# Optimization experiments

Measured on AMD Instinct MI355X. Metric: run time of the kernel, lower is better.

Reference implementation:

```python
import math
import jax, jax.numpy as jnp
import numpy as np

N = 100000
E = 3200000
NFEAT = 128
NHID = 128
NCLASS = 40
NLAYERS = 8
LAMDA = 0.5
ALPHA = 0.1


def setup_inputs() -> dict:
    key = jax.random.key(0)
    ks = jax.random.split(key, 8)
    x = jax.random.normal(ks[0], (N, NFEAT), dtype=jnp.float32)
    edge_src = jax.random.randint(ks[1], (E,), 0, N, dtype=jnp.int32)
    edge_dst = jax.random.randint(ks[2], (E,), 0, N, dtype=jnp.int32)
    # positive normalized-adjacency-like values
    edge_val = jax.random.uniform(ks[3], (E,), dtype=jnp.float32) * 0.05
    W_in = jax.random.normal(ks[4], (NFEAT, NHID), dtype=jnp.float32) * (1.0 / math.sqrt(NFEAT))
    b_in = jnp.zeros((NHID,), dtype=jnp.float32)
    conv_w = jax.random.normal(ks[5], (NLAYERS, NHID, NHID), dtype=jnp.float32) * (1.0 / math.sqrt(NHID))
    W_out = jax.random.normal(ks[6], (NHID, NCLASS), dtype=jnp.float32) * (1.0 / math.sqrt(NHID))
    b_out = jnp.zeros((NCLASS,), dtype=jnp.float32)
    return {"x": x, "edge_src": edge_src, "edge_dst": edge_dst, "edge_val": edge_val,
            "W_in": W_in, "b_in": b_in, "conv_w": conv_w, "W_out": W_out, "b_out": b_out}


def _spmm(edge_src, edge_dst, edge_val, h):
    # sparse adj @ h : gather source rows, scale by edge weight, scatter-add to dst
    msgs = edge_val[:, None] * h[edge_src]          # [E, NHID]
    return jax.ops.segment_sum(msgs, edge_dst, num_segments=N)


def reference(x, edge_src, edge_dst, edge_val, W_in, b_in, conv_w, W_out, b_out):
    h0 = x @ W_in + b_in                            # fc_in (dropout = identity in eval)
    h = h0
    for i in range(NLAYERS):
        layer_idx = i + 1
        theta = math.log(LAMDA / layer_idx + 1.0)
        hi = _spmm(edge_src, edge_dst, edge_val, h)  # [N, NHID]
        support = (1.0 - ALPHA) * hi + ALPHA * h0    # convex combine with initial residual
        out = theta * (support @ conv_w[i]) + (1.0 - theta) * support  # identity mapping mix
        h = jax.nn.relu(out)
    return h @ W_out + b_out                         # fc_out
```

## Files before the change

### kernel.cpp

```cpp
#include <hip/hip_runtime.h>
#include <hip/hip_fp16.h>


constexpr int NN = 100000;
constexpr int EE = 3200000;
constexpr int NB = 256;
constexpr int NBUCK = (NN + 511) / 512;

struct alignas(8) Half4 { __half2 lo, hi; };

__global__ __launch_bounds__(256) void bhist_kernel(const int* __restrict__ dst,
                                                    int* __restrict__ bhist, int e) {
    __shared__ int lh[NB];
    lh[threadIdx.x] = 0;
    __syncthreads();
    for (int i = blockIdx.x * 256 + threadIdx.x; i < e; i += gridDim.x * 256)
        atomicAdd(&lh[dst[i] >> 9], 1);
    __syncthreads();
    if (lh[threadIdx.x]) atomicAdd(&bhist[threadIdx.x], lh[threadIdx.x]);
}

__global__ void bscan_kernel(const int* __restrict__ bhist, int* __restrict__ bbase,
                             int* __restrict__ bcur, int* __restrict__ row_ptr) {
    if (threadIdx.x == 0) {
        int s = 0;
        for (int b = 0; b < NB; ++b) { bbase[b] = s; bcur[b] = s; s += bhist[b]; }
        bbase[NB] = s;
        row_ptr[NN] = s;
    }
}

__global__ __launch_bounds__(256, 3) void bucket_kernel(const int* __restrict__ src,
                                                        const int* __restrict__ dst,
                                                        const float* __restrict__ val,
                                                        int* __restrict__ bcur,
                                                        int2* __restrict__ bsorted,
                                                        int* __restrict__ bdst, int e_total) {
    __shared__ int bin_cnt[NB], bin_excl[NB], bin_gbase[NB], bin_cur[NB];
    __shared__ int2 s_ed[4096];
    __shared__ int  s_dp[4096];
    const int tid = threadIdx.x;
    const int e_base = blockIdx.x * 4096;
    const int count = min(4096, e_total - e_base);
    bin_cnt[tid] = 0;
    __syncthreads();
    #pragma unroll
    for (int i = 0; i < 16; ++i) {
        int idx = e_base + i * 256 + tid;
        if (idx < e_total) atomicAdd(&bin_cnt[dst[idx] >> 9], 1);
    }
    __syncthreads();
    if (tid == 0) {
        int s = 0;
        for (int b = 0; b < NB; ++b) { bin_excl[b] = s; s += bin_cnt[b]; }
    }
    __syncthreads();
    bin_gbase[tid] = atomicAdd(&bcur[tid], bin_cnt[tid]);
    bin_cur[tid] = bin_excl[tid];
    __syncthreads();
    #pragma unroll
    for (int i = 0; i < 16; ++i) {
        int idx = e_base + i * 256 + tid;
        if (idx < e_total) {
            int d = dst[idx];
            int pos = atomicAdd(&bin_cur[d >> 9], 1);
            s_ed[pos] = make_int2(src[idx], __float_as_int(val[idx]));
            s_dp[pos] = d;
        }
    }
    __syncthreads();
    for (int pos = tid; pos < count; pos += 256) {
        int d = s_dp[pos], b = d >> 9;
        int g = bin_gbase[b] + (pos - bin_excl[b]);
        bsorted[g] = s_ed[pos];
        bdst[g] = d;
    }
}

__global__ __launch_bounds__(512) void finalize_kernel(const int2* __restrict__ bsorted,
                                                       const int* __restrict__ bdst,
                                                       const int* __restrict__ bbase,
                                                       int* __restrict__ row_ptr,
                                                       int2* __restrict__ csr) {
    __shared__ int hist[512], cur[512], wsum[8];
    const int tid = threadIdx.x, lane = tid & 63, wid = tid >> 6;
    const int b = blockIdx.x;
    const int n0 = b << 9;
    const int nodes = min(512, NN - n0);
    const int es = bbase[b], ee = bbase[b + 1], cnt = ee - es;
    hist[tid] = 0;
    __syncthreads();
    for (int i = tid; i < cnt; i += 512) atomicAdd(&hist[bdst[es + i] - n0], 1);
    __syncthreads();
    int v = hist[tid];
    int x = v;
    #pragma unroll
    for (int d = 1; d < 64; d <<= 1) {
        int y = __shfl_up(x, (unsigned)d);
        if (lane >= d) x += y;
    }
    if (lane == 63) wsum[wid] = x;
    __syncthreads();
    if (tid == 0) {
        int s = 0;
        for (int w = 0; w < 8; ++w) { int t2 = wsum[w]; wsum[w] = s; s += t2; }
    }
    __syncthreads();
    int excl = x - v + wsum[wid];
    cur[tid] = excl;
    if (tid < nodes) row_ptr[n0 + tid] = es + excl;
    __syncthreads();
    for (int i = tid; i < cnt; i += 512) {
        int d = bdst[es + i];
        int p = atomicAdd(&cur[d - n0], 1);
        csr[es + p] = bsorted[es + i];
    }
}

__global__ void prep_wc_kernel(const float* __restrict__ conv_w, float* __restrict__ Wc) {
    int layer = blockIdx.y;
    int idx = blockIdx.x * 256 + threadIdx.x;
    float theta = logf(0.5f / (float)(layer + 1) + 1.0f);
    int k = idx >> 7, j = idx & 127;
    float w = conv_w[layer * 16384 + idx];
    Wc[layer * 16384 + idx] = theta * w + ((k == j) ? (1.0f - theta) : 0.0f);
}

__global__ __launch_bounds__(256, 2) void fc_in_kernel(const float* __restrict__ x,
                                                       const float* __restrict__ W,
                                                       const float* __restrict__ b,
                                                       __half* __restrict__ h0) {
    __shared__ float sW[128 * 128];
    __shared__ float sA[32 * 128];
    const int tid = threadIdx.x;
    #pragma unroll
    for (int t = 0; t < 16; ++t)
        ((float4*)sW)[t * 256 + tid] = ((const float4*)W)[t * 256 + tid];
    const float4* xs = (const float4*)(x + (size_t)blockIdx.x * 32 * 128);
    #pragma unroll
    for (int t = 0; t < 4; ++t)
        ((float4*)sA)[t * 256 + tid] = xs[t * 256 + tid];
    __syncthreads();

    const int rowg = tid >> 5, colg = tid & 31;
    float4 bias = ((const float4*)b)[colg];
    float acc[4][4];
    #pragma unroll
    for (int r = 0; r < 4; ++r) { acc[r][0] = bias.x; acc[r][1] = bias.y; acc[r][2] = bias.z; acc[r][3] = bias.w; }

    for (int k = 0; k < 128; ++k) {
        float4 w = *(const float4*)&sW[k * 128 + (colg << 2)];
        float s[4];
        #pragma unroll
        for (int r = 0; r < 4; ++r) s[r] = sA[((rowg << 2) + r) * 128 + k];
        #pragma unroll
        for (int r = 0; r < 4; ++r) {
            acc[r][0] = fmaf(s[r], w.x, acc[r][0]);
            acc[r][1] = fmaf(s[r], w.y, acc[r][1]);
            acc[r][2] = fmaf(s[r], w.z, acc[r][2]);
            acc[r][3] = fmaf(s[r], w.w, acc[r][3]);
        }
    }
    const int row0 = blockIdx.x * 32;
    #pragma unroll
    for (int r = 0; r < 4; ++r) {
        Half4 o;
        o.lo = __floats2half2_rn(acc[r][0], acc[r][1]);
        o.hi = __floats2half2_rn(acc[r][2], acc[r][3]);
        *(Half4*)(h0 + ((size_t)(row0 + (rowg << 2) + r) << 7) + (colg << 2)) = o;
    }
}

#define FMA4(ACC, PV, G) { \
    float vv_ = __int_as_float((PV).y); \
    float2 lo_ = __half22float2((G).lo), hi_ = __half22float2((G).hi); \
    (ACC).x = fmaf(vv_, lo_.x, (ACC).x); (ACC).y = fmaf(vv_, lo_.y, (ACC).y); \
    (ACC).z = fmaf(vv_, hi_.x, (ACC).z); (ACC).w = fmaf(vv_, hi_.y, (ACC).w); }

__global__ __launch_bounds__(256, 8) void layer_kernel(const __half* __restrict__ h,
                                                       const __half* __restrict__ h0,
                                                       const int2* __restrict__ csr,
                                                       const int* __restrict__ row_ptr,
                                                       const float* __restrict__ Wc,
                                                       __half* __restrict__ hn) {
    __shared__ float sS[32 * 128];
    const int tid = threadIdx.x;
    const int wid = tid >> 6, lane = tid & 63;
    const int sub = lane >> 5;
    const int q4 = (lane & 31) << 2;
    const int row0 = blockIdx.x * 32;
    const int rb = __builtin_amdgcn_readfirstlane(row0 + wid * 8);

    for (int rr = 0; rr < 8; ++rr) {
        const int r = rb + rr;
        const int e0 = row_ptr[r], e1 = row_ptr[r + 1];
        float4 accA = make_float4(0.f, 0.f, 0.f, 0.f);
        float4 accB = make_float4(0.f, 0.f, 0.f, 0.f);
        int e = e0;
        for (; e + 16 <= e1; e += 16) {
            int2 c0 = csr[e + 0],  c1 = csr[e + 1],  c2 = csr[e + 2],  c3 = csr[e + 3];
            int2 c4 = csr[e + 4],  c5 = csr[e + 5],  c6 = csr[e + 6],  c7 = csr[e + 7];
            int2 c8 = csr[e + 8],  c9 = csr[e + 9],  c10 = csr[e + 10], c11 = csr[e + 11];
            int2 c12 = csr[e + 12], c13 = csr[e + 13], c14 = csr[e + 14], c15 = csr[e + 15];
            int2 p0 = sub ? c1 : c0;
            int2 p1 = sub ? c3 : c2;
            int2 p2 = sub ? c5 : c4;
            int2 p3 = sub ? c7 : c6;
            int2 p4 = sub ? c9 : c8;
            int2 p5 = sub ? c11 : c10;
            int2 p6 = sub ? c13 : c12;
            int2 p7 = sub ? c15 : c14;
            Half4 g0 = *(const Half4*)(h + ((size_t)p0.x << 7) + q4);
            Half4 g1 = *(const Half4*)(h + ((size_t)p1.x << 7) + q4);
            Half4 g2 = *(const Half4*)(h + ((size_t)p2.x << 7) + q4);
            Half4 g3 = *(const Half4*)(h + ((size_t)p3.x << 7) + q4);
            Half4 g4 = *(const Half4*)(h + ((size_t)p4.x << 7) + q4);
            Half4 g5 = *(const Half4*)(h + ((size_t)p5.x << 7) + q4);
            Half4 g6 = *(const Half4*)(h + ((size_t)p6.x << 7) + q4);
            Half4 g7 = *(const Half4*)(h + ((size_t)p7.x << 7) + q4);
            FMA4(accA, p0, g0); FMA4(accB, p1, g1);
            FMA4(accA, p2, g2); FMA4(accB, p3, g3);
            FMA4(accA, p4, g4); FMA4(accB, p5, g5);
            FMA4(accA, p6, g6); FMA4(accB, p7, g7);
        }
        if (e < e1) {
            #pragma unroll
            for (int k = 0; k < 8; ++k) {
                int iL = e + 2 * k;
                int2 cl = csr[(iL < e1) ? iL : (e1 - 1)];
                int2 ch = csr[(iL + 1 < e1) ? (iL + 1) : (e1 - 1)];
                int2 p = sub ? ch : cl;
                if (iL + sub >= e1) p.y = 0;
                Half4 g = *(const Half4*)(h + ((size_t)p.x << 7) + q4);
                if (k & 1) { FMA4(accB, p, g); } else { FMA4(accA, p, g); }
            }
        }
        float4 acc;
        acc.x = accA.x + accB.x; acc.y = accA.y + accB.y;
        acc.z = accA.z + accB.z; acc.w = accA.w + accB.w;
        acc.x += __shfl_xor(acc.x, 32);
        acc.y += __shfl_xor(acc.y, 32);
        acc.z += __shfl_xor(acc.z, 32);
        acc.w += __shfl_xor(acc.w, 32);
        if (sub == 0) {
            Half4 q = *(const Half4*)(h0 + ((size_t)r << 7) + q4);
            float2 a = __half22float2(q.lo), c = __half22float2(q.hi);
            float4 sv;
            sv.x = 0.9f * acc.x + 0.1f * a.x;
            sv.y = 0.9f * acc.y + 0.1f * a.y;
            sv.z = 0.9f * acc.z + 0.1f * c.x;
            sv.w = 0.9f * acc.w + 0.1f * c.y;
            *(float4*)&sS[(wid * 8 + rr) * 128 + q4] = sv;
        }
    }
    __syncthreads();

    const int rowg = tid >> 5, colg = tid & 31;
    const float* wp = Wc + (colg << 2);
    float acc2[4][4] = {};
    for (int k = 0; k < 128; k += 2) {
        float4 w0 = *(const float4*)(wp + ((size_t)k << 7));
        float4 w1 = *(const float4*)(wp + ((size_t)(k + 1) << 7));
        float s0[4], s1[4];
        #pragma unroll
        for (int r = 0; r < 4; ++r) {
            s0[r] = sS[((rowg << 2) + r) * 128 + k];
            s1[r] = sS[((rowg << 2) + r) * 128 + k + 1];
        }
        #pragma unroll
        for (int r = 0; r < 4; ++r) {
            acc2[r][0] = fmaf(s0[r], w0.x, acc2[r][0]);
            acc2[r][1] = fmaf(s0[r], w0.y, acc2[r][1]);
            acc2[r][2] = fmaf(s0[r], w0.z, acc2[r][2]);
            acc2[r][3] = fmaf(s0[r], w0.w, acc2[r][3]);
            acc2[r][0] = fmaf(s1[r], w1.x, acc2[r][0]);
            acc2[r][1] = fmaf(s1[r], w1.y, acc2[r][1]);
            acc2[r][2] = fmaf(s1[r], w1.z, acc2[r][2]);
            acc2[r][3] = fmaf(s1[r], w1.w, acc2[r][3]);
        }
    }
    #pragma unroll
    for (int r = 0; r < 4; ++r) {
        Half4 o;
        o.lo = __floats2half2_rn(fmaxf(acc2[r][0], 0.f), fmaxf(acc2[r][1], 0.f));
        o.hi = __floats2half2_rn(fmaxf(acc2[r][2], 0.f), fmaxf(acc2[r][3], 0.f));
        *(Half4*)(hn + ((size_t)(row0 + (rowg << 2) + r) << 7) + (colg << 2)) = o;
    }
}

__global__ __launch_bounds__(256, 3) void fc_out_kernel(const __half* __restrict__ h,
                                                        const float* __restrict__ W,
                                                        const float* __restrict__ b,
                                                        float* __restrict__ out, int n) {
    __shared__ float sW[128 * 40];
    __shared__ float sA[64 * 128];
    const int tid = threadIdx.x;
    #pragma unroll
    for (int t = 0; t < 5; ++t)
        ((float4*)sW)[t * 256 + tid] = ((const float4*)W)[t * 256 + tid];
    const int row0 = blockIdx.x * 64;
    #pragma unroll
    for (int t = 0; t < 8; ++t) {
        int idx = t * 256 + tid;
        int row = idx >> 5;
        int gr = row0 + row;
        float4 v = make_float4(0.f, 0.f, 0.f, 0.f);
        if (gr < n) {
            Half4 q = *(const Half4*)(h + ((size_t)gr << 7) + ((idx & 31) << 2));
            float2 a = __half22float2(q.lo), c = __half22float2(q.hi);
            v = make_float4(a.x, a.y, c.x, c.y);
        }
        *(float4*)&sA[row * 128 + ((idx & 31) << 2)] = v;
    }
    __syncthreads();

    const int rowg = tid >> 3;
    const int colg = tid & 7;
    float acc[2][5];
    #pragma unroll
    for (int c = 0; c < 5; ++c) {
        float bb = b[colg * 5 + c];
        acc[0][c] = bb; acc[1][c] = bb;
    }
    for (int k = 0; k < 128; ++k) {
        float s0 = sA[(rowg * 2 + 0) * 128 + k];
        float s1 = sA[(rowg * 2 + 1) * 128 + k];
        #pragma unroll
        for (int c = 0; c < 5; ++c) {
            float w = sW[k * 40 + colg * 5 + c];
            acc[0][c] = fmaf(s0, w, acc[0][c]);
            acc[1][c] = fmaf(s1, w, acc[1][c]);
        }
    }
    #pragma unroll
    for (int rr = 0; rr < 2; ++rr) {
        int r = row0 + rowg * 2 + rr;
        if (r < n) {
            #pragma unroll
            for (int c = 0; c < 5; ++c)
                out[(size_t)r * 40 + colg * 5 + c] = acc[rr][c];
        }
    }
}

extern "C" void kernel_launch(void* const* d_in, const int* in_sizes, int n_in,
                              void* d_out, int out_size, void* d_ws, size_t ws_size,
                              hipStream_t stream) {
    const float* x      = (const float*)d_in[0];
    const int*   esrc   = (const int*)d_in[1];
    const int*   edst   = (const int*)d_in[2];
    const float* eval   = (const float*)d_in[3];
    const float* W_in   = (const float*)d_in[4];
    const float* b_in   = (const float*)d_in[5];
    const float* conv_w = (const float*)d_in[6];
    const float* W_out  = (const float*)d_in[7];
    const float* b_out  = (const float*)d_in[8];
    float* out = (float*)d_out;

    __half* h0     = (__half*)d_ws;
    __half* hA     = h0 + (size_t)NN * 128;
    __half* hB     = hA + (size_t)NN * 128;
    float*  Wc     = (float*)(hB + (size_t)NN * 128);
    int*   row_ptr = (int*)(Wc + 8 * 128 * 128);
    int*   bhist   = row_ptr + (NN + 2);
    int*   bbase   = bhist + NB;
    int*   bcur    = bbase + (NB + 2);
    int2*  csr     = (int2*)(bcur + NB);
    int2*  bsorted = csr + EE;
    int*   bdst    = (int*)(bsorted + EE);

    hipMemsetAsync(bhist, 0, NB * sizeof(int), stream);
    bhist_kernel<<<1024, 256, 0, stream>>>(edst, bhist, EE);
    bscan_kernel<<<1, 64, 0, stream>>>(bhist, bbase, bcur, row_ptr);
    bucket_kernel<<<(EE + 4095) / 4096, 256, 0, stream>>>(esrc, edst, eval, bcur,
                                                          bsorted, bdst, EE);
    finalize_kernel<<<NBUCK, 512, 0, stream>>>(bsorted, bdst, bbase, row_ptr, csr);

    prep_wc_kernel<<<dim3(64, 8), 256, 0, stream>>>(conv_w, Wc);

    fc_in_kernel<<<NN / 32, 256, 0, stream>>>(x, W_in, b_in, h0);

    const __half* hin = h0;
    __half* hout = hA;
    for (int i = 0; i < 8; ++i) {
        layer_kernel<<<NN / 32, 256, 0, stream>>>(hin, h0, csr, row_ptr, Wc + i * 16384, hout);
        hin = hout;
        hout = (hout == hA) ? hB : hA;
    }

    fc_out_kernel<<<(NN + 63) / 64, 256, 0, stream>>>(hin, W_out, b_out, out, NN);
}
```

Baseline: 1.522 ms.

## Pre-shift CSR indices to byte offsets and use packed f32x2 FMAs in layer kernel

Stores source indices in the CSR pre-multiplied by the row stride in bytes, so gathers use a 32-bit add instead of 64-bit shift and multiply address math. Each half-wave now loads only its own CSR entry rather than loading 16 and selecting. Accumulations in both the gather and the dense transform use 2-wide float vectors, so the compiler can emit packed FMA instructions. The 32-bit byte offset relies on N*256 fitting in an int, and the two FMA paths now round accumulations differently.

```diff
diff --git a/kernel.cpp b/kernel.cpp
--- a/kernel.cpp
+++ b/kernel.cpp
@@ -8,6 +8,7 @@
 constexpr int NBUCK = (NN + 511) / 512;
 
 struct alignas(8) Half4 { __half2 lo, hi; };
+typedef float f32x2 __attribute__((ext_vector_type(2)));
 
 __global__ __launch_bounds__(256) void bhist_kernel(const int* __restrict__ dst,
                                                     int* __restrict__ bhist, int e) {
@@ -113,7 +114,9 @@
     for (int i = tid; i < cnt; i += 512) {
         int d = bdst[es + i];
         int p = atomicAdd(&cur[d - n0], 1);
-        csr[es + p] = bsorted[es + i];
+        int2 ev = bsorted[es + i];
+        ev.x <<= 8;
+        csr[es + p] = ev;
     }
 }
 
@@ -171,11 +174,13 @@
     }
 }
 
-#define FMA4(ACC, PV, G) { \
-    float vv_ = __int_as_float((PV).y); \
+#define FMA4(A0, A1, PV, G) { \
+    float v_ = __int_as_float((PV).y); \
+    f32x2 vv_ = {v_, v_}; \
     float2 lo_ = __half22float2((G).lo), hi_ = __half22float2((G).hi); \
-    (ACC).x = fmaf(vv_, lo_.x, (ACC).x); (ACC).y = fmaf(vv_, lo_.y, (ACC).y); \
-    (ACC).z = fmaf(vv_, hi_.x, (ACC).z); (ACC).w = fmaf(vv_, hi_.y, (ACC).w); }
+    f32x2 gl_ = {lo_.x, lo_.y}, gh_ = {hi_.x, hi_.y}; \
+    A0 += vv_ * gl_; \
+    A1 += vv_ * gh_; }
 
 __global__ __launch_bounds__(256, 8) void layer_kernel(const __half* __restrict__ h,
                                                        const __half* __restrict__ h0,
@@ -188,62 +193,59 @@
     const int wid = tid >> 6, lane = tid & 63;
     const int sub = lane >> 5;
     const int q4 = (lane & 31) << 2;
+    const int q4b = q4 << 1;
+    const char* hb = (const char*)h;
+    const char* h0b = (const char*)h0;
     const int row0 = blockIdx.x * 32;
     const int rb = __builtin_amdgcn_readfirstlane(row0 + wid * 8);
 
     for (int rr = 0; rr < 8; ++rr) {
         const int r = rb + rr;
         const int e0 = row_ptr[r], e1 = row_ptr[r + 1];
-        float4 accA = make_float4(0.f, 0.f, 0.f, 0.f);
-        float4 accB = make_float4(0.f, 0.f, 0.f, 0.f);
+        f32x2 aA0 = {0.f, 0.f}, aA1 = {0.f, 0.f};
+        f32x2 aB0 = {0.f, 0.f}, aB1 = {0.f, 0.f};
         int e = e0;
         for (; e + 16 <= e1; e += 16) {
-            int2 c0 = csr[e + 0],  c1 = csr[e + 1],  c2 = csr[e + 2],  c3 = csr[e + 3];
-            int2 c4 = csr[e + 4],  c5 = csr[e + 5],  c6 = csr[e + 6],  c7 = csr[e + 7];
-            int2 c8 = csr[e + 8],  c9 = csr[e + 9],  c10 = csr[e + 10], c11 = csr[e + 11];
-            int2 c12 = csr[e + 12], c13 = csr[e + 13], c14 = csr[e + 14], c15 = csr[e + 15];
-            int2 p0 = sub ? c1 : c0;
-            int2 p1 = sub ? c3 : c2;
-            int2 p2 = sub ? c5 : c4;
-            int2 p3 = sub ? c7 : c6;
-            int2 p4 = sub ? c9 : c8;
-            int2 p5 = sub ? c11 : c10;
-            int2 p6 = sub ? c13 : c12;
-            int2 p7 = sub ? c15 : c14;
-            Half4 g0 = *(const Half4*)(h + ((size_t)p0.x << 7) + q4);
-            Half4 g1 = *(const Half4*)(h + ((size_t)p1.x << 7) + q4);
-            Half4 g2 = *(const Half4*)(h + ((size_t)p2.x << 7) + q4);
-            Half4 g3 = *(const Half4*)(h + ((size_t)p3.x << 7) + q4);
-            Half4 g4 = *(const Half4*)(h + ((size_t)p4.x << 7) + q4);
-            Half4 g5 = *(const Half4*)(h + ((size_t)p5.x << 7) + q4);
-            Half4 g6 = *(const Half4*)(h + ((size_t)p6.x << 7) + q4);
-            Half4 g7 = *(const Half4*)(h + ((size_t)p7.x << 7) + q4);
-            FMA4(accA, p0, g0); FMA4(accB, p1, g1);
-            FMA4(accA, p2, g2); FMA4(accB, p3, g3);
-            FMA4(accA, p4, g4); FMA4(accB, p5, g5);
-            FMA4(accA, p6, g6); FMA4(accB, p7, g7);
+            int2 p0 = csr[e + sub + 0];
+            int2 p1 = csr[e + sub + 2];
+            int2 p2 = csr[e + sub + 4];
+            int2 p3 = csr[e + sub + 6];
+            int2 p4 = csr[e + sub + 8];
+            int2 p5 = csr[e + sub + 10];
+            int2 p6 = csr[e + sub + 12];
+            int2 p7 = csr[e + sub + 14];
+            Half4 g0 = *(const Half4*)(hb + (unsigned)(p0.x + q4b));
+            Half4 g1 = *(const Half4*)(hb + (unsigned)(p1.x + q4b));
+            Half4 g2 = *(const Half4*)(hb + (unsigned)(p2.x + q4b));
+            Half4 g3 = *(const Half4*)(hb + (unsigned)(p3.x + q4b));
+            Half4 g4 = *(const Half4*)(hb + (unsigned)(p4.x + q4b));
+            Half4 g5 = *(const Half4*)(hb + (unsigned)(p5.x + q4b));
+            Half4 g6 = *(const Half4*)(hb + (unsigned)(p6.x + q4b));
+            Half4 g7 = *(const Half4*)(hb + (unsigned)(p7.x + q4b));
+            FMA4(aA0, aA1, p0, g0); FMA4(aB0, aB1, p1, g1);
+            FMA4(aA0, aA1, p2, g2); FMA4(aB0, aB1, p3, g3);
+            FMA4(aA0, aA1, p4, g4); FMA4(aB0, aB1, p5, g5);
+            FMA4(aA0, aA1, p6, g6); FMA4(aB0, aB1, p7, g7);
         }
         if (e < e1) {
             #pragma unroll
             for (int k = 0; k < 8; ++k) {
-                int iL = e + 2 * k;
-                int2 cl = csr[(iL < e1) ? iL : (e1 - 1)];
-                int2 ch = csr[(iL + 1 < e1) ? (iL + 1) : (e1 - 1)];
-                int2 p = sub ? ch : cl;
-                if (iL + sub >= e1) p.y = 0;
-                Half4 g = *(const Half4*)(h + ((size_t)p.x << 7) + q4);
-                if (k & 1) { FMA4(accB, p, g); } else { FMA4(accA, p, g); }
+                int idx = e + 2 * k + sub;
+                int2 p = csr[(idx < e1) ? idx : (e1 - 1)];
+                if (idx >= e1) p.y = 0;
+                Half4 g = *(const Half4*)(hb + (unsigned)(p.x + q4b));
+                if (k & 1) { FMA4(aB0, aB1, p, g); }
+                else       { FMA4(aA0, aA1, p, g); }
             }
         }
-        float4 acc;
-        acc.x = accA.x + accB.x; acc.y = accA.y + accB.y;
-        acc.z = accA.z + accB.z; acc.w = accA.w + accB.w;
+        f32x2 a0 = aA0 + aB0, a1 = aA1 + aB1;
+        float4 acc = make_float4(a0.x, a0.y, a1.x, a1.y);
         acc.x += __shfl_xor(acc.x, 32);
         acc.y += __shfl_xor(acc.y, 32);
         acc.z += __shfl_xor(acc.z, 32);
         acc.w += __shfl_xor(acc.w, 32);
         if (sub == 0) {
-            Half4 q = *(const Half4*)(h0 + ((size_t)r << 7) + q4);
+            Half4 q = *(const Half4*)(h0b + ((size_t)r << 8) + q4b);
             float2 a = __half22float2(q.lo), c = __half22float2(q.hi);
             float4 sv;
             sv.x = 0.9f * acc.x + 0.1f * a.x;
@@ -257,33 +259,28 @@
 
     const int rowg = tid >> 5, colg = tid & 31;
     const float* wp = Wc + (colg << 2);
-    float acc2[4][4] = {};
+    f32x2 acc2[4][2] = {};
     for (int k = 0; k < 128; k += 2) {
         float4 w0 = *(const float4*)(wp + ((size_t)k << 7));
         float4 w1 = *(const float4*)(wp + ((size_t)(k + 1) << 7));
-        float s0[4], s1[4];
+        f32x2 w0a = {w0.x, w0.y}, w0b = {w0.z, w0.w};
+        f32x2 w1a = {w1.x, w1.y}, w1b = {w1.z, w1.w};
         #pragma unroll
         for (int r = 0; r < 4; ++r) {
-            s0[r] = sS[((rowg << 2) + r) * 128 + k];
-            s1[r] = sS[((rowg << 2) + r) * 128 + k + 1];
-        }
-        #pragma unroll
-        for (int r = 0; r < 4; ++r) {
-            acc2[r][0] = fmaf(s0[r], w0.x, acc2[r][0]);
-            acc2[r][1] = fmaf(s0[r], w0.y, acc2[r][1]);
-            acc2[r][2] = fmaf(s0[r], w0.z, acc2[r][2]);
-            acc2[r][3] = fmaf(s0[r], w0.w, acc2[r][3]);
-            acc2[r][0] = fmaf(s1[r], w1.x, acc2[r][0]);
-            acc2[r][1] = fmaf(s1[r], w1.y, acc2[r][1]);
-            acc2[r][2] = fmaf(s1[r], w1.z, acc2[r][2]);
-            acc2[r][3] = fmaf(s1[r], w1.w, acc2[r][3]);
+            float s0 = sS[((rowg << 2) + r) * 128 + k];
+            float s1 = sS[((rowg << 2) + r) * 128 + k + 1];
+            f32x2 s0v = {s0, s0}, s1v = {s1, s1};
+            acc2[r][0] += s0v * w0a;
+            acc2[r][1] += s0v * w0b;
+            acc2[r][0] += s1v * w1a;
+            acc2[r][1] += s1v * w1b;
         }
     }
     #pragma unroll
     for (int r = 0; r < 4; ++r) {
         Half4 o;
-        o.lo = __floats2half2_rn(fmaxf(acc2[r][0], 0.f), fmaxf(acc2[r][1], 0.f));
-        o.hi = __floats2half2_rn(fmaxf(acc2[r][2], 0.f), fmaxf(acc2[r][3], 0.f));
+        o.lo = __floats2half2_rn(fmaxf(acc2[r][0].x, 0.f), fmaxf(acc2[r][0].y, 0.f));
+        o.hi = __floats2half2_rn(fmaxf(acc2[r][1].x, 0.f), fmaxf(acc2[r][1].y, 0.f));
         *(Half4*)(hn + ((size_t)(row0 + (rowg << 2) + r) << 7) + (colg << 2)) = o;
     }
 }
```

After: 1.712 ms. 12.5% more time.
